# Kernel optimization log

Hardware: AMD Instinct MI355X
Metric: run time of the kernel (lower is better)

The kernel has to match this reference:

```python
import jax, jax.numpy as jnp
import numpy as np

N = 100000        # num_nodes
W_IN = 256        # input feature dim
W_OUT = 64        # args.node_dim
C = 2             # args.num_channels
T = 4             # num_edge_type
E = 800000        # edges per edge type
NUM_CLASS = 4
M = 20000         # number of target nodes
BETA = 0.5        # args.beta


def setup_inputs() -> dict:
    key = jax.random.key(0)
    ks = jax.random.split(key, 10)
    X = jax.random.normal(ks[0], (N, W_IN), dtype=jnp.float32)
    edge_index = jax.random.randint(ks[1], (T, 2, E), 0, N)
    edge_value = jax.random.uniform(ks[2], (T, E), dtype=jnp.float32)
    target_x = jax.random.randint(ks[3], (M,), 0, N)
    target = jax.random.randint(ks[4], (M,), 0, NUM_CLASS)
    # learned params
    Ws = jax.random.normal(ks[5], (C, W_IN, W_OUT), dtype=jnp.float32) * 0.05   # GCNConv weights
    conv_weight = jax.random.normal(ks[6], (C, T), dtype=jnp.float32) * 0.1     # FastGTConv.weight
    linear1_W = jax.random.normal(ks[7], (W_OUT, W_OUT * C), dtype=jnp.float32) * 0.05
    linear1_b = jnp.zeros((W_OUT,), dtype=jnp.float32)
    lin_W = jax.random.normal(ks[8], (NUM_CLASS, W_OUT), dtype=jnp.float32) * 0.05
    lin_b = jnp.zeros((NUM_CLASS,), dtype=jnp.float32)
    return dict(X=X, edge_value=edge_value, Ws=Ws, conv_weight=conv_weight,
                linear1_W=linear1_W, linear1_b=linear1_b, lin_W=lin_W, lin_b=lin_b,
                edge_index=edge_index, target_x=target_x, target=target)


def reference(X, edge_value, Ws, conv_weight, linear1_W, linear1_b, lin_W, lin_b,
              edge_index, target_x, target):
    # FastGTConv: softmax over edge types per channel
    filt = jax.nn.softmax(conv_weight, axis=1)            # [C, T]
    rows = edge_index[:, 0, :].reshape(-1)                # [T*E]
    cols = edge_index[:, 1, :].reshape(-1)                # [T*E]
    # X_ = H = [X @ W_c for each channel]
    X_ = jnp.einsum('nd,cdo->cno', X, Ws)                 # [C, N, W_OUT]
    outs = []
    for c in range(C):
        # concat+coalesce(add) then spmm == scatter-add of weighted messages
        vals = (edge_value * filt[c][:, None]).reshape(-1)       # [T*E]
        msgs = vals[:, None] * X_[c][cols]                        # [T*E, W_OUT]
        Hc = jax.ops.segment_sum(msgs, rows, num_segments=N)      # [N, W_OUT]
        outs.append(jax.nn.relu(BETA * X_[c] + (1.0 - BETA) * Hc))
    H_ = jnp.concatenate(outs, axis=1)                    # [N, C*W_OUT]
    H_ = jax.nn.relu(H_ @ linear1_W.T + linear1_b)        # [N, W_OUT]
    y = H_[target_x] @ lin_W.T + lin_b                    # [M, NUM_CLASS]
    logp = jax.nn.log_softmax(y, axis=-1)
    loss = -jnp.mean(jnp.take_along_axis(logp, target[:, None], axis=1))
    return loss, y
```

## Files before the change

### kernel.cpp

```cpp
#include <hip/hip_runtime.h>

#define N_NODES 100000
#define W_INF   256
#define W_OUTF  64
#define C_CH    2
#define T_ET    4
#define E_EDGE  800000
#define NUM_CLS 4
#define M_TGT   20000
#define BETA    0.5f
#define MAXDEG  96

typedef __attribute__((ext_vector_type(8))) short bf16x8;
typedef __attribute__((ext_vector_type(4))) float floatx4;

__device__ inline short f2bf(float f) {
    unsigned u = __builtin_bit_cast(unsigned, f);
    u += 0x7FFF + ((u >> 16) & 1);
    return (short)(u >> 16);
}
__device__ inline float bflo(unsigned q) { return __builtin_bit_cast(float, q << 16); }
__device__ inline float bfhi(unsigned q) { return __builtin_bit_cast(float, q & 0xFFFF0000u); }

__global__ void setup_kernel(const float* __restrict__ Ws,
                             const float* __restrict__ conv_weight,
                             const int* __restrict__ target_x,
                             short* __restrict__ Bt, float* __restrict__ filt,
                             int* __restrict__ rid, int* __restrict__ nrows,
                             float* __restrict__ out) {
    int i = blockIdx.x * 256 + threadIdx.x;
    if (i == 0) { *nrows = 0; out[0] = 0.f; }
    if (i < C_CH) {
        int c = i;
        float mx = -1e30f;
        for (int t = 0; t < T_ET; t++) mx = fmaxf(mx, conv_weight[c * T_ET + t]);
        float e[T_ET];
        float s = 0.f;
        for (int t = 0; t < T_ET; t++) { e[t] = expf(conv_weight[c * T_ET + t] - mx); s += e[t]; }
        for (int t = 0; t < T_ET; t++) filt[c * T_ET + t] = e[t] / s;
    }
    if (i < C_CH * W_OUTF * W_INF) {
        int co = i >> 8, k = i & 255;
        int c = co >> 6, o = co & 63;
        Bt[i] = f2bf(Ws[((size_t)c * W_INF + k) * W_OUTF + o]);
    }
    if (i < M_TGT) rid[target_x[i]] = -2;
}

__global__ void compact_kernel(int* __restrict__ rid, int* __restrict__ row_list,
                               int* __restrict__ nrows, int* __restrict__ counts) {
    int n = blockIdx.x * blockDim.x + threadIdx.x;
    if (n < M_TGT) counts[n] = 0;
    int lane = threadIdx.x & 63;
    bool flag = (n < N_NODES) && (rid[n] == -2);
    unsigned long long mask = __ballot(flag);
    int base = 0;
    if (lane == 0 && mask) base = atomicAdd(nrows, __popcll(mask));
    base = __shfl(base, 0);
    if (flag) {
        int id = base + __popcll(mask & ((1ULL << lane) - 1ULL));
        rid[n] = id;
        row_list[id] = n;
    }
}

#define GMT  64
#define BLDA2 136
#define GEMM_NB  ((N_NODES + GMT - 1) / GMT)
#define BUILD_BX ((E_EDGE / 8 + 255) / 256)
#define BUILD_TOT (BUILD_BX * T_ET)
__global__ __launch_bounds__(256, 4)
void fused_gemm_build(const float* __restrict__ X, const short* __restrict__ Bt,
                      short* __restrict__ Xp,
                      const int* __restrict__ edge_index,
                      const float* __restrict__ edge_value,
                      const int* __restrict__ rid,
                      int* __restrict__ counts,
                      unsigned long long* __restrict__ records) {
    __shared__ short Bl[64][BLDA2];
    int tid = threadIdx.x;
    int bx = blockIdx.x;
    if ((bx & 1) == 0) {
        int g = bx >> 1;
        if (g >= GEMM_NB) return;
        int w = tid >> 6, lane = tid & 63;
        int quad = lane >> 4, l15 = lane & 15;
        int m0 = g * GMT + w * 16;
        int arow = m0 + l15;
        if (arow >= N_NODES) arow = N_NODES - 1;
        const float* xrow = X + (size_t)arow * W_INF;
        floatx4 acc[C_CH][4] = {};
        #pragma unroll 1
        for (int kh = 0; kh < 2; kh++) {
            bf16x8 af[4];
            #pragma unroll
            for (int kc = 0; kc < 4; kc++) {
                int kb = kh * 128 + kc * 32 + quad * 8;
                float4 v0 = *(const float4*)&xrow[kb];
                float4 v1 = *(const float4*)&xrow[kb + 4];
                af[kc][0] = f2bf(v0.x); af[kc][1] = f2bf(v0.y);
                af[kc][2] = f2bf(v0.z); af[kc][3] = f2bf(v0.w);
                af[kc][4] = f2bf(v1.x); af[kc][5] = f2bf(v1.y);
                af[kc][6] = f2bf(v1.z); af[kc][7] = f2bf(v1.w);
            }
            #pragma unroll
            for (int c = 0; c < C_CH; c++) {
                if (kh | c) __syncthreads();
                #pragma unroll
                for (int l = 0; l < 4; l++) {
                    int idx = tid + l * 256;
                    int r = idx >> 4;
                    int kp = (idx & 15) * 8;
                    *(bf16x8*)&Bl[r][kp] =
                        *(const bf16x8*)&Bt[(size_t)(c * 64 + r) * W_INF + kh * 128 + kp];
                }
                __syncthreads();
                #pragma unroll
                for (int kc = 0; kc < 4; kc++) {
                    int kb = kc * 32 + quad * 8;
                    #pragma unroll
                    for (int nt = 0; nt < 4; nt++) {
                        bf16x8 b = *(bf16x8*)&Bl[nt * 16 + l15][kb];
                        acc[c][nt] =
                            __builtin_amdgcn_mfma_f32_16x16x32_bf16(af[kc], b, acc[c][nt], 0, 0, 0);
                    }
                }
            }
        }
        #pragma unroll
        for (int nt = 0; nt < 4; nt++) {
            int o = nt * 16 + l15;
            #pragma unroll
            for (int r = 0; r < 4; r++) {
                int m = m0 + quad * 4 + r;
                if (m < N_NODES) {
                    unsigned pk = (unsigned)(unsigned short)f2bf(acc[0][nt][r])
                                | ((unsigned)(unsigned short)f2bf(acc[1][nt][r]) << 16);
                    *(unsigned*)&Xp[(size_t)m * (C_CH * W_OUTF) + o * 2] = pk;
                }
            }
        }
    } else {
        int bb = bx >> 1;
        if (bb >= BUILD_TOT) return;
        int t = bb / BUILD_BX;
        int i = (bb - t * BUILD_BX) * 256 + tid;
        if (i >= E_EDGE / 8) return;
        int e = i * 8;
        const int*   rbase = &edge_index[(size_t)(t * 2 + 0) * E_EDGE + e];
        const int*   cbase = &edge_index[(size_t)(t * 2 + 1) * E_EDGE + e];
        const float* vbase = &edge_value[(size_t)t * E_EDGE + e];
        int4   r4a = *(const int4*)  &rbase[0], r4b = *(const int4*)  &rbase[4];
        int4   c4a = *(const int4*)  &cbase[0], c4b = *(const int4*)  &cbase[4];
        float4 v4a = *(const float4*)&vbase[0], v4b = *(const float4*)&vbase[4];
        int rows[8] = {r4a.x, r4a.y, r4a.z, r4a.w, r4b.x, r4b.y, r4b.z, r4b.w};
        int cols[8] = {c4a.x, c4a.y, c4a.z, c4a.w, c4b.x, c4b.y, c4b.z, c4b.w};
        float evv[8] = {v4a.x, v4a.y, v4a.z, v4a.w, v4b.x, v4b.y, v4b.z, v4b.w};
        int ids[8];
        #pragma unroll
        for (int j = 0; j < 8; j++) ids[j] = rid[rows[j]];
        #pragma unroll
        for (int j = 0; j < 8; j++) {
            if (ids[j] >= 0) {
                int p = atomicAdd(&counts[ids[j]], 1);
                if (p < MAXDEG) {
                    unsigned long long rec =
                        (unsigned long long)(unsigned)(cols[j] | (t << 20)) |
                        ((unsigned long long)__float_as_uint(evv[j]) << 32);
                    records[(size_t)ids[j] * MAXDEG + p] = rec;
                }
            }
        }
    }
}

#define GROWS 8
__device__ __forceinline__ void process_row(
    int n, int cnt, unsigned long long rl, unsigned long long rh,
    const unsigned* __restrict__ xb, const float (*w1s)[W_OUTF],
    const float* f0, const float* f1, float bias, int lane,
    float lw0, float lw1, float lw2, float lw3,
    float lb0, float lb1, float lb2, float lb3,
    float4* __restrict__ yv, int b)
{
    unsigned rl_lo = (unsigned)rl, rl_hi = (unsigned)(rl >> 32);
    unsigned rh_lo = (unsigned)rh, rh_hi = (unsigned)(rh >> 32);
    float a0 = 0.f, a1 = 0.f, a0b = 0.f, a1b = 0.f;
    int nb = (cnt + 15) & ~15;
    for (int p = 0; p < nb; p += 16) {
        unsigned blo = (p < 64) ? rl_lo : rh_lo;
        unsigned bhi = (p < 64) ? rl_hi : rh_hi;
        int poff = (p < 64) ? p : p - 64;
        unsigned klo[16], khi[16], q[16];
        #pragma unroll
        for (int j = 0; j < 16; j++) {
            klo[j] = __shfl(blo, poff + j);
            khi[j] = __shfl(bhi, poff + j);
        }
        #pragma unroll
        for (int j = 0; j < 16; j++)
            q[j] = xb[(size_t)(klo[j] & 0xFFFFF) * 64];
        #pragma unroll
        for (int j = 0; j < 16; j += 2) {
            int ta = (int)(klo[j] >> 20), tb = (int)(klo[j + 1] >> 20);
            float ea = __uint_as_float(khi[j]), eb = __uint_as_float(khi[j + 1]);
            a0  += ea * f0[ta] * bflo(q[j]);
            a1  += ea * f1[ta] * bfhi(q[j]);
            a0b += eb * f0[tb] * bflo(q[j + 1]);
            a1b += eb * f1[tb] * bfhi(q[j + 1]);
        }
    }
    a0 += a0b; a1 += a1b;
    unsigned qn = xb[(size_t)n * 64];
    float hc0 = fmaxf(BETA * bflo(qn) + (1.f - BETA) * a0, 0.f);
    float hc1 = fmaxf(BETA * bfhi(qn) + (1.f - BETA) * a1, 0.f);
    float s0 = bias, s1 = 0.f, s2 = 0.f, s3 = 0.f;
    #pragma unroll
    for (int k = 0; k < W_OUTF; k += 4) {
        s0 += __shfl(hc0, k)     * w1s[k][lane ^ (k & 31)];
        s1 += __shfl(hc0, k + 1) * w1s[k + 1][lane ^ ((k + 1) & 31)];
        s2 += __shfl(hc0, k + 2) * w1s[k + 2][lane ^ ((k + 2) & 31)];
        s3 += __shfl(hc0, k + 3) * w1s[k + 3][lane ^ ((k + 3) & 31)];
    }
    #pragma unroll
    for (int k = 0; k < W_OUTF; k += 4) {
        s0 += __shfl(hc1, k)     * w1s[W_OUTF + k][lane ^ (k & 31)];
        s1 += __shfl(hc1, k + 1) * w1s[W_OUTF + k + 1][lane ^ ((k + 1) & 31)];
        s2 += __shfl(hc1, k + 2) * w1s[W_OUTF + k + 2][lane ^ ((k + 2) & 31)];
        s3 += __shfl(hc1, k + 3) * w1s[W_OUTF + k + 3][lane ^ ((k + 3) & 31)];
    }
    float h2 = fmaxf((s0 + s1) + (s2 + s3), 0.f);
    float p0 = lw0 * h2, p1 = lw1 * h2, p2 = lw2 * h2, p3 = lw3 * h2;
    #pragma unroll
    for (int off = 32; off > 0; off >>= 1) {
        p0 += __shfl_xor(p0, off);
        p1 += __shfl_xor(p1, off);
        p2 += __shfl_xor(p2, off);
        p3 += __shfl_xor(p3, off);
    }
    if (lane == 0)
        yv[b] = make_float4(p0 + lb0, p1 + lb1, p2 + lb2, p3 + lb3);
}

__global__ void gather_kernel(const int* __restrict__ row_list,
                              const int* __restrict__ counts,
                              const unsigned long long* __restrict__ records,
                              const float* __restrict__ filt,
                              const short* __restrict__ Xp,
                              const float* __restrict__ W1,
                              const float* __restrict__ b1,
                              const float* __restrict__ linW,
                              const float* __restrict__ linb,
                              float4* __restrict__ yv,
                              const int* __restrict__ nrows_ptr) {
    __shared__ float w1s[C_CH * W_OUTF][W_OUTF];
    int tid = threadIdx.x;
    for (int i = tid; i < W_OUTF * C_CH * W_OUTF; i += 256) {
        int o = i >> 7, k = i & 127;
        w1s[k][o ^ (k & 31)] = W1[i];
    }
    __syncthreads();
    int w = tid >> 6, lane = tid & 63;
    int nrows = *nrows_ptr;
    float f0[T_ET], f1[T_ET];
    #pragma unroll
    for (int t = 0; t < T_ET; t++) { f0[t] = filt[t]; f1[t] = filt[T_ET + t]; }
    float bias = b1[lane];
    float lw0 = linW[0 * W_OUTF + lane], lw1 = linW[1 * W_OUTF + lane];
    float lw2 = linW[2 * W_OUTF + lane], lw3 = linW[3 * W_OUTF + lane];
    float lb0 = linb[0], lb1 = linb[1], lb2 = linb[2], lb3 = linb[3];
    const unsigned* xb = (const unsigned*)Xp + lane;

    int b0 = blockIdx.x * GROWS + w;
    int b1r = b0 + 4;
    bool v0 = b0 < nrows, v1 = b1r < nrows;
    int n0 = 0, c0 = 0, n1 = 0, c1 = 0;
    unsigned long long rl0 = 0, rh0 = 0, rl1 = 0, rh1 = 0;
    if (v0) {
        n0 = row_list[b0];
        c0 = counts[b0]; if (c0 > MAXDEG) c0 = MAXDEG;
        const unsigned long long* rec = records + (size_t)b0 * MAXDEG;
        rl0 = (lane < c0)      ? rec[lane]      : 0ULL;
        rh0 = (lane + 64 < c0) ? rec[lane + 64] : 0ULL;
    }
    if (v1) {
        n1 = row_list[b1r];
        c1 = counts[b1r]; if (c1 > MAXDEG) c1 = MAXDEG;
        const unsigned long long* rec = records + (size_t)b1r * MAXDEG;
        rl1 = (lane < c1)      ? rec[lane]      : 0ULL;
        rh1 = (lane + 64 < c1) ? rec[lane + 64] : 0ULL;
    }
    if (v0) process_row(n0, c0, rl0, rh0, xb, w1s, f0, f1, bias, lane,
                        lw0, lw1, lw2, lw3, lb0, lb1, lb2, lb3, yv, b0);
    if (v1) process_row(n1, c1, rl1, rh1, xb, w1s, f0, f1, bias, lane,
                        lw0, lw1, lw2, lw3, lb0, lb1, lb2, lb3, yv, b1r);
}

__global__ void loss_kernel(const float4* __restrict__ yv,
                            const int* __restrict__ rid,
                            const int* __restrict__ target_x,
                            const int* __restrict__ target,
                            float* __restrict__ out) {
    __shared__ float loss_s[4];
    int tid = threadIdx.x;
    int wave = tid >> 6, lane = tid & 63;
    int m = blockIdx.x * 256 + tid;
    float l = 0.f;
    if (m < M_TGT) {
        int id = rid[target_x[m]];
        float4 y = yv[id];
        *(float4*)&out[1 + (size_t)m * NUM_CLS] = y;
        float mx = fmaxf(fmaxf(y.x, y.y), fmaxf(y.z, y.w));
        float s = expf(y.x - mx) + expf(y.y - mx) + expf(y.z - mx) + expf(y.w - mx);
        float lse = mx + logf(s);
        int tg = target[m];
        float ytg = (tg == 0) ? y.x : (tg == 1) ? y.y : (tg == 2) ? y.z : y.w;
        l = lse - ytg;
    }
    #pragma unroll
    for (int off = 32; off > 0; off >>= 1) l += __shfl_xor(l, off);
    if (lane == 0) loss_s[wave] = l;
    __syncthreads();
    if (tid == 0) {
        float L = loss_s[0] + loss_s[1] + loss_s[2] + loss_s[3];
        atomicAdd(&out[0], L * (1.0f / (float)M_TGT));
    }
}

extern "C" void kernel_launch(void* const* d_in, const int* in_sizes, int n_in,
                              void* d_out, int out_size, void* d_ws, size_t ws_size,
                              hipStream_t stream) {
    const float* X           = (const float*)d_in[0];
    const float* edge_value  = (const float*)d_in[1];
    const float* Ws          = (const float*)d_in[2];
    const float* conv_weight = (const float*)d_in[3];
    const float* linear1_W   = (const float*)d_in[4];
    const float* linear1_b   = (const float*)d_in[5];
    const float* lin_W       = (const float*)d_in[6];
    const float* lin_b       = (const float*)d_in[7];
    const int*   edge_index  = (const int*)d_in[8];
    const int*   target_x    = (const int*)d_in[9];
    const int*   target      = (const int*)d_in[10];
    float* out = (float*)d_out;

    char* ws = (char*)d_ws;
    size_t off = 0;
    float* filt  = (float*)(ws + off); off += 256;
    size_t xbytes = (size_t)N_NODES * C_CH * W_OUTF * sizeof(short);
    short* Xp    = (short*)(ws + off); off += xbytes;
    float4* yv   = (float4*)(ws + off); off += (size_t)M_TGT * sizeof(float4);
    unsigned long long* records = (unsigned long long*)(ws + off);
    off += (size_t)M_TGT * MAXDEG * sizeof(unsigned long long);
    short* Bt    = (short*)(ws + off); off += (size_t)C_CH * W_OUTF * W_INF * sizeof(short);
    int*   rid   = (int*)  (ws + off); off += (size_t)N_NODES * sizeof(int);
    int*   row_list = (int*)(ws + off); off += (size_t)M_TGT * sizeof(int);
    int*   counts   = (int*)(ws + off); off += (size_t)M_TGT * sizeof(int);
    int*   nrows    = (int*)(ws + off); off += 256;

    hipMemsetAsync(rid, 0xFF, (size_t)N_NODES * sizeof(int), stream);

    setup_kernel<<<128, 256, 0, stream>>>(Ws, conv_weight, target_x, Bt, filt, rid, nrows, out);
    compact_kernel<<<(N_NODES + 255) / 256, 256, 0, stream>>>(rid, row_list, nrows, counts);
    fused_gemm_build<<<2 * BUILD_TOT, 256, 0, stream>>>(
        X, Bt, Xp, edge_index, edge_value, rid, counts, records);
    gather_kernel<<<(M_TGT + GROWS - 1) / GROWS, 256, 0, stream>>>(
        row_list, counts, records, filt, Xp, linear1_W, linear1_b,
        lin_W, lin_b, yv, nrows);
    loss_kernel<<<(M_TGT + 255) / 256, 256, 0, stream>>>(yv, rid, target_x, target, out);
}
```

Measured before the change: 304.0 us.

## Use persistent gather blocks with atomic work queue and record prefetch

The gather kernel now launches a fixed grid of persistent blocks, and each wave takes rows from a global atomic counter instead of a static two-rows-per-wave mapping. The records for the next row are loaded before the current row is processed, which overlaps record fetch latency with compute. This aims to balance uneven row degrees and cut per-block W1 shared-memory staging overhead. The cost is one global atomic per row and extra registers for the prefetched state.

```diff
diff --git a/kernel.cpp b/kernel.cpp
--- a/kernel.cpp
+++ b/kernel.cpp
@@ -29,7 +29,7 @@
                              int* __restrict__ rid, int* __restrict__ nrows,
                              float* __restrict__ out) {
     int i = blockIdx.x * 256 + threadIdx.x;
-    if (i == 0) { *nrows = 0; out[0] = 0.f; }
+    if (i == 0) { nrows[0] = 0; nrows[1] = 0; out[0] = 0.f; }
     if (i < C_CH) {
         int c = i;
         float mx = -1e30f;
@@ -174,7 +174,7 @@
     }
 }
 
-#define GROWS 8
+#define GQ_BLOCKS 1280
 __device__ __forceinline__ void process_row(
     int n, int cnt, unsigned long long rl, unsigned long long rh,
     const unsigned* __restrict__ xb, const float (*w1s)[W_OUTF],
@@ -242,17 +242,18 @@
         yv[b] = make_float4(p0 + lb0, p1 + lb1, p2 + lb2, p3 + lb3);
 }
 
-__global__ void gather_kernel(const int* __restrict__ row_list,
-                              const int* __restrict__ counts,
-                              const unsigned long long* __restrict__ records,
-                              const float* __restrict__ filt,
-                              const short* __restrict__ Xp,
-                              const float* __restrict__ W1,
-                              const float* __restrict__ b1,
-                              const float* __restrict__ linW,
-                              const float* __restrict__ linb,
-                              float4* __restrict__ yv,
-                              const int* __restrict__ nrows_ptr) {
+__global__ __launch_bounds__(256)
+void gather_kernel(const int* __restrict__ row_list,
+                   const int* __restrict__ counts,
+                   const unsigned long long* __restrict__ records,
+                   const float* __restrict__ filt,
+                   const short* __restrict__ Xp,
+                   const float* __restrict__ W1,
+                   const float* __restrict__ b1,
+                   const float* __restrict__ linW,
+                   const float* __restrict__ linb,
+                   float4* __restrict__ yv,
+                   int* __restrict__ nrows_ptr) {
     __shared__ float w1s[C_CH * W_OUTF][W_OUTF];
     int tid = threadIdx.x;
     for (int i = tid; i < W_OUTF * C_CH * W_OUTF; i += 256) {
@@ -260,8 +261,8 @@
         w1s[k][o ^ (k & 31)] = W1[i];
     }
     __syncthreads();
-    int w = tid >> 6, lane = tid & 63;
-    int nrows = *nrows_ptr;
+    int lane = tid & 63;
+    int nrows = nrows_ptr[0];
     float f0[T_ET], f1[T_ET];
     #pragma unroll
     for (int t = 0; t < T_ET; t++) { f0[t] = filt[t]; f1[t] = filt[T_ET + t]; }
@@ -271,29 +272,35 @@
     float lb0 = linb[0], lb1 = linb[1], lb2 = linb[2], lb3 = linb[3];
     const unsigned* xb = (const unsigned*)Xp + lane;
 
-    int b0 = blockIdx.x * GROWS + w;
-    int b1r = b0 + 4;
-    bool v0 = b0 < nrows, v1 = b1r < nrows;
-    int n0 = 0, c0 = 0, n1 = 0, c1 = 0;
-    unsigned long long rl0 = 0, rh0 = 0, rl1 = 0, rh1 = 0;
-    if (v0) {
-        n0 = row_list[b0];
-        c0 = counts[b0]; if (c0 > MAXDEG) c0 = MAXDEG;
-        const unsigned long long* rec = records + (size_t)b0 * MAXDEG;
-        rl0 = (lane < c0)      ? rec[lane]      : 0ULL;
-        rh0 = (lane + 64 < c0) ? rec[lane + 64] : 0ULL;
-    }
-    if (v1) {
-        n1 = row_list[b1r];
-        c1 = counts[b1r]; if (c1 > MAXDEG) c1 = MAXDEG;
-        const unsigned long long* rec = records + (size_t)b1r * MAXDEG;
-        rl1 = (lane < c1)      ? rec[lane]      : 0ULL;
-        rh1 = (lane + 64 < c1) ? rec[lane + 64] : 0ULL;
-    }
-    if (v0) process_row(n0, c0, rl0, rh0, xb, w1s, f0, f1, bias, lane,
-                        lw0, lw1, lw2, lw3, lb0, lb1, lb2, lb3, yv, b0);
-    if (v1) process_row(n1, c1, rl1, rh1, xb, w1s, f0, f1, bias, lane,
-                        lw0, lw1, lw2, lw3, lb0, lb1, lb2, lb3, yv, b1r);
+    int cur = 0;
+    if (lane == 0) cur = atomicAdd(&nrows_ptr[1], 1);
+    cur = __shfl(cur, 0);
+    int n_c = 0, c_c = 0;
+    unsigned long long rl_c = 0, rh_c = 0;
+    if (cur < nrows) {
+        n_c = row_list[cur];
+        c_c = counts[cur]; if (c_c > MAXDEG) c_c = MAXDEG;
+        const unsigned long long* rec = records + (size_t)cur * MAXDEG;
+        rl_c = (lane < c_c)      ? rec[lane]      : 0ULL;
+        rh_c = (lane + 64 < c_c) ? rec[lane + 64] : 0ULL;
+    }
+    while (cur < nrows) {
+        int nxt = 0;
+        if (lane == 0) nxt = atomicAdd(&nrows_ptr[1], 1);
+        nxt = __shfl(nxt, 0);
+        int n_n = 0, c_n = 0;
+        unsigned long long rl_n = 0, rh_n = 0;
+        if (nxt < nrows) {
+            n_n = row_list[nxt];
+            c_n = counts[nxt]; if (c_n > MAXDEG) c_n = MAXDEG;
+            const unsigned long long* rec = records + (size_t)nxt * MAXDEG;
+            rl_n = (lane < c_n)      ? rec[lane]      : 0ULL;
+            rh_n = (lane + 64 < c_n) ? rec[lane + 64] : 0ULL;
+        }
+        process_row(n_c, c_c, rl_c, rh_c, xb, w1s, f0, f1, bias, lane,
+                    lw0, lw1, lw2, lw3, lb0, lb1, lb2, lb3, yv, cur);
+        cur = nxt; n_c = n_n; c_c = c_n; rl_c = rl_n; rh_c = rh_n;
+    }
 }
 
 __global__ void loss_kernel(const float4* __restrict__ yv,
@@ -363,7 +370,7 @@
     compact_kernel<<<(N_NODES + 255) / 256, 256, 0, stream>>>(rid, row_list, nrows, counts);
     fused_gemm_build<<<2 * BUILD_TOT, 256, 0, stream>>>(
         X, Bt, Xp, edge_index, edge_value, rid, counts, records);
-    gather_kernel<<<(M_TGT + GROWS - 1) / GROWS, 256, 0, stream>>>(
+    gather_kernel<<<GQ_BLOCKS, 256, 0, stream>>>(
         row_list, counts, records, filt, Xp, linear1_W, linear1_b,
         lin_W, lin_b, yv, nrows);
     loss_kernel<<<(M_TGT + 255) / 256, 256, 0, stream>>>(yv, rid, target_x, target, out);
```

Measured after the change: 511.4 us. +68.2%, slower.
